# Kernel optimization log

Hardware: AMD Instinct MI355X
Metric: run time of the kernel (lower is better)

The kernel has to match this reference:

```python
import jax, jax.numpy as jnp
import numpy as np

CM = 8        # channel_mult
EPS = 1e-5    # BatchNorm eps
NEG = 0.2     # LeakyReLU slope


def conv2d(x, w, stride, pad, b=None):
    y = jax.lax.conv_general_dilated(
        x, w, (stride, stride), [(pad, pad), (pad, pad)],
        dimension_numbers=('NCHW', 'OIHW', 'NCHW'))
    if b is not None:
        y = y + b[None, :, None, None]
    return y


def per_sample_conv(x, w, stride, pad):
    # x: [B,C,H,W], w: [B,O,C,kh,kw] -> per-sample conv, vmapped over batch
    f = lambda xi, wi: conv2d(xi[None], wi, stride, pad)[0]
    return jax.vmap(f)(x, w)


def batchnorm(x, g, b):
    # training-mode BN: batch statistics over (N,H,W)
    m = jnp.mean(x, axis=(0, 2, 3), keepdims=True)
    v = jnp.var(x, axis=(0, 2, 3), keepdims=True)
    return (x - m) * jax.lax.rsqrt(v + EPS) * g[None, :, None, None] + b[None, :, None, None]


def lrelu(x):
    return jnp.where(x >= 0, x, NEG * x)


def setup_inputs() -> dict:
    key = jax.random.key(0)
    ks = jax.random.split(key, 16)
    B, H, W = 16, 512, 512

    def rn(k, shape, fan_in):
        return jax.random.normal(k, shape, jnp.float32) * np.float32(1.0 / np.sqrt(fan_in))

    inp = {}
    inp['x'] = jax.random.normal(ks[0], (B, 3, H, W), jnp.float32)
    n_meta = 3 * (CM // 2) * 25 + CM * (CM * 2 // 2) * 25  # 300 + 1600 = 1900
    inp['conv_weights'] = jax.random.normal(ks[1], (B, n_meta), jnp.float32) * 0.05
    inp['w11'] = rn(ks[2], (CM // 2, 3, 5, 5), 3 * 25)
    inp['b11'] = jnp.zeros((CM // 2,), jnp.float32)
    inp['w12'] = rn(ks[3], (CM * 2 // 2, CM, 5, 5), CM * 25)
    inp['b12'] = jnp.zeros((CM * 2 // 2,), jnp.float32)
    inp['bn1_g'] = jnp.ones((CM * 2,), jnp.float32)
    inp['bn1_b'] = jnp.zeros((CM * 2,), jnp.float32)
    # conv2 stack: (in, out, kernel)
    chans = [(CM * 2, CM * 4, 5), (CM * 4, CM * 8, 5), (CM * 8, CM * 16, 3), (CM * 16, CM * 16, 3)]
    for i, (ci, co, k) in enumerate(chans, 1):
        inp[f'c2w{i}'] = rn(ks[3 + i], (co, ci, k, k), ci * k * k)
        inp[f'c2b{i}'] = jnp.zeros((co,), jnp.float32)
        inp[f'bn{i}g'] = jnp.ones((co,), jnp.float32)
        inp[f'bn{i}b'] = jnp.zeros((co,), jnp.float32)
    return inp


def reference(x, conv_weights, w11, b11, w12, b12, bn1_g, bn1_b,
              c2w1, c2b1, bn1g, bn1b, c2w2, c2b2, bn2g, bn2b,
              c2w3, c2b3, bn3g, bn3b, c2w4, c2b4, bn4g, bn4b):
    B, _, H, W = x.shape
    n1 = 3 * (CM // 2) * 25
    w1 = conv_weights[:, :n1].reshape(B, CM // 2, 3, 5, 5)
    w2 = conv_weights[:, n1:].reshape(B, CM * 2 // 2, CM, 5, 5)

    # meta layer 1: shared half + per-sample dynamic half
    xx = conv2d(x, w11, 1, 2, b11)                  # [B, cm/2, H, W]
    half = per_sample_conv(x, w1, 1, 2)             # [B, cm/2, H, W]
    h = lrelu(jnp.concatenate([xx, half], axis=1))  # [B, cm, H, W]

    # meta layer 2 (stride 2)
    xx = conv2d(h, w12, 2, 2, b12)                  # [B, cm, H/2, W/2]
    half = per_sample_conv(h, w2, 2, 2)             # [B, cm, H/2, W/2]
    h = lrelu(batchnorm(jnp.concatenate([xx, half], axis=1), bn1_g, bn1_b))

    # dense conv stack
    for w_, b_, g_, be_, p in [
        (c2w1, c2b1, bn1g, bn1b, 2),
        (c2w2, c2b2, bn2g, bn2b, 2),
        (c2w3, c2b3, bn3g, bn3b, 1),
        (c2w4, c2b4, bn4g, bn4b, 1),
    ]:
        h = lrelu(batchnorm(conv2d(h, w_, 2, p, b_), g_, be_))

    return h.reshape(-1, CM * 16, H // 32, W // 32)
```

## Files before the change

kernel.cpp:

```cpp
#include <hip/hip_runtime.h>


typedef __attribute__((ext_vector_type(8))) short short8v;
typedef __attribute__((ext_vector_type(4))) float float4v;
typedef unsigned short u16;

#define LRELU_NEG 0.2f
#define BN_EPS 1e-5f

__device__ __forceinline__ float bf2f(u16 u){ union{unsigned i; float f;} v; v.i=(unsigned)u<<16; return v.f; }
__device__ __forceinline__ u16 f2bf(float f){ unsigned x=__float_as_uint(f); x += 0x7FFFu + ((x>>16)&1u); return (u16)(x>>16); }
__device__ __forceinline__ float lrelu(float v){ return v<0.f? LRELU_NEG*v : v; }

__device__ __forceinline__ void packw(int i, const float* __restrict__ w, u16* __restrict__ dst,
                                      int IC, int OC, int KSZ, int CPR) {
  int kq = i & 31, oc = (i>>5) % OC, c = i/(OC*32);
  int ky = c / CPR, r = c % CPR;
  int kk = r*32 + kq; int kx = kk / IC, ic = kk % IC;
  float v = (kx < KSZ) ? w[(((size_t)oc*IC + ic)*KSZ + ky)*KSZ + kx] : 0.f;
  dst[i] = f2bf(v);
}

__global__ __launch_bounds__(256) void prep_all(
    const float* __restrict__ w11, const float* __restrict__ w12,
    const float* __restrict__ b12, const float* __restrict__ cw,
    const float* __restrict__ wc1, const float* __restrict__ wc2,
    const float* __restrict__ wc3, const float* __restrict__ wc4,
    u16* __restrict__ wl1d, u16* __restrict__ wl2m, float* __restrict__ bl2,
    u16* __restrict__ d1, u16* __restrict__ d2, u16* __restrict__ d3, u16* __restrict__ d4,
    u16* __restrict__ h1) {
  int i = blockIdx.x*256 + threadIdx.x;
  if (i < 16) {
    bl2[i] = (i<8)? b12[i] : 0.f;
  } else if (i < 49168) {
    int j = i - 16;
    int b = j / 3072, r = j % 3072;
    int c = r >> 9, r2 = r & 511;
    int row = r2 >> 5, kk = r2 & 31;
    int kx = kk >> 2, ic = kk & 3;
    int grp = row >> 3, oc = row & 7;
    int ky = c - grp;
    float v = 0.f;
    if (ic < 3 && kx < 5 && ky >= 0 && ky < 5)
      v = (oc < 4) ? w11[((oc*3+ic)*5+ky)*5+kx]
                   : cw[b*1900 + (oc-4)*75 + ic*25 + ky*5 + kx];
    wl1d[j] = f2bf(v);
  } else if (i < 131088) {
    int j = i - 49168;
    int kq = j & 31, oc = (j>>5) & 15, c = (j>>9) % 10, b = j / 5120;
    int ky = c >> 1, r = c & 1;
    int kk = r*32 + kq; int kx = kk >> 3, ic = kk & 7;
    float v = 0.f;
    if (kx < 5)
      v = (oc < 8) ? w12[((oc*8+ic)*5+ky)*5+kx]
                   : cw[b*1900 + 300 + ((oc-8)*8+ic)*25 + ky*5 + kx];
    wl2m[j] = f2bf(v);
  } else if (i < 196880) {
    int j = i - 131088;
    int b = j / 4112, p = j % 4112;
    int y, xx;
    if (p < 2064) { int r = p/516; y = (r<2)? r : 512+r; xx = p%516; }
    else          { int q = p-2064; int cidx = q&3; xx = (cidx<2)? cidx : 512+cidx; y = 2 + (q>>2); }
    short8v z = {0,0,0,0,0,0,0,0};
    *(short8v*)(h1 + ((((size_t)b*516 + y)*2 + (xx&1))*258 + (xx>>1))*8) = z;
  } else if (i < 484624) {
    int j = i - 196880;
    if (j < 15360) packw(j, wc1, d1, 16, 32, 5, 3);
    else if (j < 66560) packw(j-15360, wc2, d2, 32, 64, 5, 5);
    else if (j < 140288) packw(j-66560, wc3, d3, 64, 128, 3, 6);
    else packw(j-140288, wc4, d4, 128, 128, 3, 12);
  }
}

__global__ __launch_bounds__(256) void conv_l1(const float* __restrict__ x,
    const u16* __restrict__ wl1d, const float* __restrict__ b11,
    u16* __restrict__ h1) {
  __shared__ __align__(16) u16 sx[20*72*4 + 32];
  const int tid = threadIdx.x, b = blockIdx.z;
  const int x0 = (blockIdx.x & 7) * 64;
  const int r0 = (blockIdx.x >> 3) * 16;

  if (tid < 32) sx[20*72*4 + tid] = 0;

  const bool interior = (r0 >= 16) & (r0 <= 480) & (x0 >= 64) & (x0 <= 384);
  if (interior) {
    for (int e = tid; e < 360; e += 256) {
      int row = e / 18, cg = e % 18;
      size_t base = ((size_t)b*3*512 + r0 + row - 2)*512 + x0 + cg*4 - 4;
      float4v p0 = *(const float4v*)(x + base);
      float4v p1 = *(const float4v*)(x + base + 262144);
      float4v p2 = *(const float4v*)(x + base + 524288);
      short8v lo, hi;
#pragma unroll
      for (int j = 0; j < 2; j++) {
        lo[4*j+0] = (short)f2bf(p0[j]);   lo[4*j+1] = (short)f2bf(p1[j]);
        lo[4*j+2] = (short)f2bf(p2[j]);   lo[4*j+3] = 0;
        hi[4*j+0] = (short)f2bf(p0[j+2]); hi[4*j+1] = (short)f2bf(p1[j+2]);
        hi[4*j+2] = (short)f2bf(p2[j+2]); hi[4*j+3] = 0;
      }
      u16* dp = sx + (row*72 + cg*4)*4;
      *(short8v*)dp = lo;
      *(short8v*)(dp + 8) = hi;
    }
  } else {
    for (int e = tid; e < 1440; e += 256) {
      int row = e / 72, col = e % 72;
      int gy = r0 + row - 2, gx = x0 + col - 4;
      float v0 = 0.f, v1 = 0.f, v2 = 0.f;
      if (gy >= 0 && gy < 512 && gx >= 0 && gx < 512) {
        size_t base = ((size_t)b*3*512 + gy)*512 + gx;
        v0 = x[base]; v1 = x[base + 262144]; v2 = x[base + 524288];
      }
      ushort4 pk = {f2bf(v0), f2bf(v1), f2bf(v2), 0};
      *(ushort4*)(sx + e*4) = pk;
    }
  }
  __syncthreads();

  const int lane = tid & 63, w = tid >> 6;
  const int l15 = lane & 15, sub = lane >> 4;

  short8v Wf[6];
  const u16* wb = wl1d + (size_t)b*3072;
#pragma unroll
  for (int c = 0; c < 6; c++)
    Wf[c] = *(const short8v*)(wb + (c*16 + l15)*32 + sub*8);

  float bvv[4];
#pragma unroll
  for (int r = 0; r < 4; r++) bvv[r] = (sub & 1) ? 0.f : b11[r];

  const int colb = w*16 + l15;
  const int rsel = sub >> 1;
  const int x_out = x0 + colb + 2;
  const int xpar = x_out & 1, xp = x_out >> 1;

#pragma unroll
  for (int p = 0; p < 8; p++) {
    float4v acc = {0.f, 0.f, 0.f, 0.f};
#pragma unroll
    for (int c = 0; c < 6; c++) {
      const u16* ap = sx + (((2*p + c)*72 + colb + 2) << 2) + sub*8;
      union { unsigned long long q[2]; short8v v; } ua;
      ua.q[0] = *(const unsigned long long*)(ap);
      ua.q[1] = *(const unsigned long long*)(ap + 4);
      acc = __builtin_amdgcn_mfma_f32_16x16x32_bf16(Wf[c], ua.v, acc, 0, 0, 0);
    }
    union { unsigned long long q; u16 h[4]; } mine;
#pragma unroll
    for (int r = 0; r < 4; r++) mine.h[r] = f2bf(lrelu(acc[r] + bvv[r]));
    unsigned long long other = __shfl_xor((long long)mine.q, 16);
    if (!(sub & 1)) {
      int outrow = r0 + 2*p + rsel;
      u16* dst = h1 + ((((size_t)b*516 + outrow + 2)*2 + xpar)*258 + xp)*8;
      union { unsigned long long q[2]; short8v v; } pk;
      pk.q[0] = mine.q; pk.q[1] = other;
      *(short8v*)dst = pk.v;
    }
  }
}

#define LOADC(cc, Ax, Bx) do {                                                   \
    const int ky_ = (cc) / CPR, r_ = (cc) % CPR;                                 \
    const int kk0_ = r_*32 + sub*8;                                              \
    const int kx_ = kk0_ / IC, ico_ = kk0_ % IC;                                 \
    const int t_ = kx_ + PADOFF;                                                 \
    _Pragma("unroll") for (int n_ = 0; n_ < WN; n_++)                            \
      Bx[n_] = *(const short8v*)(wbase + ((size_t)(cc)*OC + oc0 + n_*16 + l15)*32 + sub*8); \
    _Pragma("unroll") for (int f_ = 0; f_ < WM; f_++) {                          \
      int iy_ = 2*oyf[f_] + ky_ + PADOFF;                                        \
      Ax[f_] = *(const short8v*)(inb + (((size_t)iy_*2 + (t_&1))*IPWH + axb[f_] + (t_>>1))*IC + ico_); \
    }                                                                            \
  } while(0)

#define MFMAC(Ax, Bx) do {                                                       \
    _Pragma("unroll") for (int f_ = 0; f_ < WM; f_++)                            \
      _Pragma("unroll") for (int n_ = 0; n_ < WN; n_++)                          \
        acc[f_][n_] = __builtin_amdgcn_mfma_f32_16x16x32_bf16(Ax[f_], Bx[n_], acc[f_][n_], 0, 0, 0); \
  } while(0)

template <int IC, int OC, int KSZ, int S, int P, int CPR, int NCH,
          int IPH, int IPW, int OWL, int OPH, int OPW,
          int WM, int WN, int WVM, int WVN, bool PERS>
__global__ __launch_bounds__(WVM*WVN*64) void conv_mfma(
    const u16* __restrict__ in, const u16* __restrict__ wmfma,
    const float* __restrict__ bias, u16* __restrict__ out,
    float2* __restrict__ part2) {
  constexpr int OW = 1 << OWL;
  constexpr int PADOFF = 2 - P;
  constexpr int IPWH = IPW / 2;
  constexpr int OPWH = OPW / 2;
  const int tid = threadIdx.x, lane = tid & 63;
  const int w = tid >> 6, wm = w % WVM, wn = w / WVM;
  const int l15 = lane & 15, sub = lane >> 4;
  const int b = blockIdx.z;
  const int px0 = blockIdx.x * (16*WM*WVM) + wm * (16*WM);
  const int oc0 = blockIdx.y * (16*WN*WVN) + wn * (16*WN);

  int oyf[WM], oxb[WM], axb[WM];
#pragma unroll
  for (int f = 0; f < WM; f++) {
    int p = px0 + f*16;
    oyf[f] = p >> OWL;
    oxb[f] = p & (OW-1);
    axb[f] = oxb[f] + l15;
  }
  const u16* inb = in + (size_t)b*IPH*IPW*IC;
  const u16* wbase = wmfma + (PERS ? (size_t)b*NCH*OC*32 : (size_t)0);

  float4v acc[WM][WN];
#pragma unroll
  for (int f = 0; f < WM; f++)
#pragma unroll
    for (int n = 0; n < WN; n++) acc[f][n] = (float4v){0.f,0.f,0.f,0.f};

  constexpr int NC = KSZ * CPR;
  short8v A0[WM], B0[WN], A1[WM], B1[WN];
  LOADC(0, A0, B0);
#pragma unroll
  for (int c = 0; c < NC; c += 2) {
    if (c + 1 < NC) LOADC(c + 1, A1, B1);
    MFMAC(A0, B0);
    if (c + 2 < NC) LOADC(c + 2, A0, B0);
    if (c + 1 < NC) MFMAC(A1, B1);
  }

  float s[WN], q[WN];
#pragma unroll
  for (int n = 0; n < WN; n++) { s[n] = 0.f; q[n] = 0.f; }
#pragma unroll
  for (int f = 0; f < WM; f++) {
    const int oxs = oxb[f] + sub*4;
    const size_t rowb2 = ((size_t)b*OPH + oyf[f] + 2)*2;
#pragma unroll
    for (int n = 0; n < WN; n++) {
      int oc = oc0 + n*16 + l15;
      float bv = bias[oc];
#pragma unroll
      for (int rr = 0; rr < 4; rr++) {
        float v = acc[f][n][rr] + bv;
        int x_out = oxs + rr + 2;
        out[((rowb2 + (x_out & 1))*OPWH + (x_out >> 1))*OC + oc] = f2bf(v);
        s[n] += v; q[n] += v*v;
      }
    }
  }
#pragma unroll
  for (int n = 0; n < WN; n++) {
    s[n] += __shfl_xor(s[n], 16); s[n] += __shfl_xor(s[n], 32);
    q[n] += __shfl_xor(q[n], 16); q[n] += __shfl_xor(q[n], 32);
  }
  __shared__ float sred[WVM*WVN][WN][16][2];
  if (sub == 0) {
#pragma unroll
    for (int n = 0; n < WN; n++) { sred[w][n][l15][0] = s[n]; sred[w][n][l15][1] = q[n]; }
  }
  __syncthreads();
  const int NBp = gridDim.x * gridDim.z;
  const int pb = blockIdx.z * gridDim.x + blockIdx.x;
  const int tot = WVN*WN*16;
  if (tid < tot) {
    int c16 = tid & 15, n = (tid >> 4) % WN, wn2 = tid / (16*WN);
    float S_ = 0.f, Q_ = 0.f;
    for (int wm2 = 0; wm2 < WVM; wm2++) {
      S_ += sred[wn2*WVM + wm2][n][c16][0];
      Q_ += sred[wn2*WVM + wm2][n][c16][1];
    }
    int c = blockIdx.y*(16*WN*WVN) + wn2*(16*WN) + n*16 + c16;
    part2[(size_t)c*NBp + pb] = make_float2(S_, Q_);
  }
}

__global__ void bn_stage2(const float2* __restrict__ part2, const float* __restrict__ g,
                          const float* __restrict__ bb, float* __restrict__ stats,
                          int NBp, float invN) {
  int c = blockIdx.x;
  float s = 0.f, q = 0.f;
  for (int i = threadIdx.x; i < NBp; i += 64) {
    float2 p = part2[(size_t)c*NBp + i];
    s += p.x; q += p.y;
  }
  for (int o = 32; o > 0; o >>= 1) { s += __shfl_down(s, o); q += __shfl_down(q, o); }
  if (threadIdx.x == 0) {
    float m = s * invN;
    float var = q * invN - m*m;
    float sc = g[c] * rsqrtf(var + BN_EPS);
    stats[2*c] = sc;
    stats[2*c+1] = bb[c] - m*sc;
  }
}

template <int C, int PH, int PW, int HH, int WW>
__global__ __launch_bounds__(256) void bn_fin(u16* __restrict__ y, const float* __restrict__ stats,
                                              int total8) {
  int i = blockIdx.x*256 + threadIdx.x;
  if (i >= total8) return;
  size_t e = (size_t)i*8;
  int c0 = (int)(e & (C-1));
  int px = (int)(e / C);
  int xp = px % (PW/2);
  int t2 = px / (PW/2);
  int yy = (t2 >> 1) % PH;
  bool interior = (yy >= 2) & (yy < 2+HH) & (xp >= 1) & (xp <= WW/2);
  short8v u = *(short8v*)(y + e);
  short8v o;
#pragma unroll
  for (int j = 0; j < 8; j++) {
    float v = bf2f((u16)u[j]) * stats[2*(c0+j)] + stats[2*(c0+j)+1];
    o[j] = interior ? (short)f2bf(lrelu(v)) : (short)0;
  }
  *(short8v*)(y + e) = o;
}

__global__ __launch_bounds__(256) void out_k(const u16* __restrict__ y6,
                                             const float* __restrict__ stats,
                                             float* __restrict__ out) {
  int i = blockIdx.x*256 + threadIdx.x;
  if (i >= 131072) return;
  size_t e = (size_t)i*4;
  int c0 = (int)(e & 127);
  int px = (int)(e >> 7);
  int loc = px & 255, b = px >> 8;
  int y = loc >> 4, x = loc & 15;
  int xi = x + 2;
  const u16* src = y6 + ((((size_t)b*20 + y + 2)*2 + (xi & 1))*10 + (xi >> 1))*128 + c0;
  ushort4 u = *(const ushort4*)src;
  float vv[4] = {bf2f(u.x), bf2f(u.y), bf2f(u.z), bf2f(u.w)};
#pragma unroll
  for (int j = 0; j < 4; j++) {
    int c = c0 + j;
    float v = vv[j] * stats[2*c] + stats[2*c+1];
    out[(((size_t)b*128 + c) << 8) + loc] = lrelu(v);
  }
}

extern "C" void kernel_launch(void* const* d_in, const int* in_sizes, int n_in,
                              void* d_out, int out_size, void* d_ws, size_t ws_size,
                              hipStream_t stream) {
  const float* x    = (const float*)d_in[0];
  const float* cw   = (const float*)d_in[1];
  const float* w11  = (const float*)d_in[2];
  const float* b11  = (const float*)d_in[3];
  const float* w12  = (const float*)d_in[4];
  const float* b12  = (const float*)d_in[5];
  const float* bn1g = (const float*)d_in[6];
  const float* bn1b = (const float*)d_in[7];
  const float* c2w[4] = {(const float*)d_in[8], (const float*)d_in[12],
                         (const float*)d_in[16], (const float*)d_in[20]};
  const float* c2b[4] = {(const float*)d_in[9], (const float*)d_in[13],
                         (const float*)d_in[17], (const float*)d_in[21]};
  const float* bng[4] = {(const float*)d_in[10], (const float*)d_in[14],
                         (const float*)d_in[18], (const float*)d_in[22]};
  const float* bnb[4] = {(const float*)d_in[11], (const float*)d_in[15],
                         (const float*)d_in[19], (const float*)d_in[23]};

  char* ws = (char*)d_ws;
  u16* h1   = (u16*)(ws);
  u16* y3   = (u16*)(ws);
  u16* y4   = (u16*)(ws + 17842176);
  u16* y5   = (u16*)(ws + 27312128);
  u16* y6   = (u16*)(ws + 32620544);
  u16* yT2  = (u16*)(ws + 68158464);
  u16* wl2m = (u16*)(ws + 102769664);
  float* bl2    = (float*)(ws + 102933504);
  float2* part2 = (float2*)(ws + 102933568);
  float* stats2 = (float*)(ws + 103457856);
  float* stats3 = stats2 + 32;
  float* stats4 = stats3 + 64;
  float* stats5 = stats4 + 128;
  float* stats6 = stats5 + 256;
  u16* wl1d = (u16*)(ws + 103460800);
  u16* wS1  = (u16*)(ws + 103559104);
  u16* wS2  = (u16*)(ws + 103589824);
  u16* wS3  = (u16*)(ws + 103692224);
  u16* wS4  = (u16*)(ws + 103839680);

  prep_all<<<1894, 256, 0, stream>>>(w11, w12, b12, cw,
                                     c2w[0], c2w[1], c2w[2], c2w[3],
                                     wl1d, wl2m, bl2, wS1, wS2, wS3, wS4, h1);

  conv_l1<<<dim3(256, 1, 16), 256, 0, stream>>>(x, wl1d, b11, h1);

  conv_mfma<8,16,5,2,2, 2,10, 516,516, 8, 260,260, 4,1,4,1, true>
      <<<dim3(256,1,16), 256, 0, stream>>>(h1, wl2m, bl2, yT2, part2);

  bn_stage2<<<16, 64, 0, stream>>>(part2, bn1g, bn1b, stats2, 4096, 1.f/1048576.f);
  bn_fin<16,260,260,256,256><<<8450, 256, 0, stream>>>(yT2, stats2, 2163200);

  conv_mfma<16,32,5,2,2, 3,15, 260,260, 7, 132,132, 2,2,4,1, false>
      <<<dim3(128,1,16), 256, 0, stream>>>(yT2, wS1, c2b[0], y3, part2);
  bn_stage2<<<32, 64, 0, stream>>>(part2, bng[0], bnb[0], stats3, 2048, 1.f/262144.f);
  bn_fin<32,132,132,128,128><<<4356, 256, 0, stream>>>(y3, stats3, 1115136);

  conv_mfma<32,64,5,2,2, 5,25, 132,132, 6, 68,68, 2,2,2,2, false>
      <<<dim3(64,1,16), 256, 0, stream>>>(y3, wS2, c2b[1], y4, part2);
  bn_stage2<<<64, 64, 0, stream>>>(part2, bng[1], bnb[1], stats4, 1024, 1.f/65536.f);
  bn_fin<64,68,68,64,64><<<2312, 256, 0, stream>>>(y4, stats4, 591872);

  conv_mfma<64,128,3,2,1, 6,18, 68,68, 5, 36,36, 2,2,2,2, false>
      <<<dim3(16,2,16), 256, 0, stream>>>(y4, wS3, c2b[2], y5, part2);
  bn_stage2<<<128, 64, 0, stream>>>(part2, bng[2], bnb[2], stats5, 256, 1.f/16384.f);
  bn_fin<128,36,36,32,32><<<1296, 256, 0, stream>>>(y5, stats5, 331776);

  conv_mfma<128,128,3,2,1, 12,36, 36,36, 4, 20,20, 2,2,1,2, false>
      <<<dim3(8,2,16), 128, 0, stream>>>(y5, wS4, c2b[3], y6, part2);
  bn_stage2<<<128, 64, 0, stream>>>(part2, bng[3], bnb[3], stats6, 128, 1.f/4096.f);

  out_k<<<512, 256, 0, stream>>>(y6, stats6, (float*)d_out);
}
```

Measured before the change: 252.2 us.

## Fuse meta conv layers 1 and 2 into one kernel via shared-memory h1 tile

Merges the first per-sample conv and the stride-2 second conv into a single kernel. Each block computes a halo-padded 36x80 tile of the 8-channel layer-1 activation in LDS and consumes it directly for layer 2, also producing the BN partial sums. This removes the full-resolution h1 round trip through global memory, one launch, and the padding-zero pass in prep. In exchange it recomputes halo rows and columns of layer 1 and uses more LDS per 512-thread block, which may lower occupancy.

```diff
diff --git a/kernel.cpp b/kernel.cpp
--- a/kernel.cpp
+++ b/kernel.cpp
@@ -27,8 +27,7 @@
     const float* __restrict__ wc1, const float* __restrict__ wc2,
     const float* __restrict__ wc3, const float* __restrict__ wc4,
     u16* __restrict__ wl1d, u16* __restrict__ wl2m, float* __restrict__ bl2,
-    u16* __restrict__ d1, u16* __restrict__ d2, u16* __restrict__ d3, u16* __restrict__ d4,
-    u16* __restrict__ h1) {
+    u16* __restrict__ d1, u16* __restrict__ d2, u16* __restrict__ d3, u16* __restrict__ d4) {
   int i = blockIdx.x*256 + threadIdx.x;
   if (i < 16) {
     bl2[i] = (i<8)? b12[i] : 0.f;
@@ -55,16 +54,8 @@
       v = (oc < 8) ? w12[((oc*8+ic)*5+ky)*5+kx]
                    : cw[b*1900 + 300 + ((oc-8)*8+ic)*25 + ky*5 + kx];
     wl2m[j] = f2bf(v);
-  } else if (i < 196880) {
+  } else if (i < 418832) {
     int j = i - 131088;
-    int b = j / 4112, p = j % 4112;
-    int y, xx;
-    if (p < 2064) { int r = p/516; y = (r<2)? r : 512+r; xx = p%516; }
-    else          { int q = p-2064; int cidx = q&3; xx = (cidx<2)? cidx : 512+cidx; y = 2 + (q>>2); }
-    short8v z = {0,0,0,0,0,0,0,0};
-    *(short8v*)(h1 + ((((size_t)b*516 + y)*2 + (xx&1))*258 + (xx>>1))*8) = z;
-  } else if (i < 484624) {
-    int j = i - 196880;
     if (j < 15360) packw(j, wc1, d1, 16, 32, 5, 3);
     else if (j < 66560) packw(j-15360, wc2, d2, 32, 64, 5, 5);
     else if (j < 140288) packw(j-66560, wc3, d3, 64, 128, 3, 6);
@@ -72,21 +63,24 @@
   }
 }
 
-__global__ __launch_bounds__(256) void conv_l1(const float* __restrict__ x,
+__global__ __launch_bounds__(512) void conv_l12(const float* __restrict__ x,
     const u16* __restrict__ wl1d, const float* __restrict__ b11,
-    u16* __restrict__ h1) {
-  __shared__ __align__(16) u16 sx[20*72*4 + 32];
+    const u16* __restrict__ wl2m, const float* __restrict__ bl2,
+    u16* __restrict__ yT2, float2* __restrict__ part2) {
+  __shared__ __align__(16) u16 sx[40*88*4];
+  __shared__ __align__(16) u16 sh1[36*2*40*8];
+  __shared__ float sred[8][16][2];
+
   const int tid = threadIdx.x, b = blockIdx.z;
-  const int x0 = (blockIdx.x & 7) * 64;
-  const int r0 = (blockIdx.x >> 3) * 16;
-
-  if (tid < 32) sx[20*72*4 + tid] = 0;
-
-  const bool interior = (r0 >= 16) & (r0 <= 480) & (x0 >= 64) & (x0 <= 384);
+  const int tx = blockIdx.x & 7, ty = blockIdx.x >> 3;
+  const int x0 = tx*32, y0 = ty*16;
+  const int xg0 = 2*x0 - 4, yg0 = 2*y0 - 4;
+
+  const bool interior = (xg0 >= 0) & (xg0 + 87 < 512) & (yg0 >= 0) & (yg0 + 39 < 512);
   if (interior) {
-    for (int e = tid; e < 360; e += 256) {
-      int row = e / 18, cg = e % 18;
-      size_t base = ((size_t)b*3*512 + r0 + row - 2)*512 + x0 + cg*4 - 4;
+    for (int e = tid; e < 880; e += 512) {
+      int row = e / 22, cg = e % 22;
+      size_t base = ((size_t)b*3*512 + yg0 + row)*512 + xg0 + cg*4;
       float4v p0 = *(const float4v*)(x + base);
       float4v p1 = *(const float4v*)(x + base + 262144);
       float4v p2 = *(const float4v*)(x + base + 524288);
@@ -98,14 +92,14 @@
         hi[4*j+0] = (short)f2bf(p0[j+2]); hi[4*j+1] = (short)f2bf(p1[j+2]);
         hi[4*j+2] = (short)f2bf(p2[j+2]); hi[4*j+3] = 0;
       }
-      u16* dp = sx + (row*72 + cg*4)*4;
+      u16* dp = sx + (row*88 + cg*4)*4;
       *(short8v*)dp = lo;
       *(short8v*)(dp + 8) = hi;
     }
   } else {
-    for (int e = tid; e < 1440; e += 256) {
-      int row = e / 72, col = e % 72;
-      int gy = r0 + row - 2, gx = x0 + col - 4;
+    for (int e = tid; e < 3520; e += 512) {
+      int row = e / 88, col = e % 88;
+      int gy = yg0 + row, gx = xg0 + col;
       float v0 = 0.f, v1 = 0.f, v2 = 0.f;
       if (gy >= 0 && gy < 512 && gx >= 0 && gx < 512) {
         size_t base = ((size_t)b*3*512 + gy)*512 + gx;
@@ -117,46 +111,92 @@
   }
   __syncthreads();
 
-  const int lane = tid & 63, w = tid >> 6;
+  const int lane = tid & 63, wid = tid >> 6;
   const int l15 = lane & 15, sub = lane >> 4;
 
-  short8v Wf[6];
-  const u16* wb = wl1d + (size_t)b*3072;
-#pragma unroll
-  for (int c = 0; c < 6; c++)
-    Wf[c] = *(const short8v*)(wb + (c*16 + l15)*32 + sub*8);
-
-  float bvv[4];
-#pragma unroll
-  for (int r = 0; r < 4; r++) bvv[r] = (sub & 1) ? 0.f : b11[r];
-
-  const int colb = w*16 + l15;
-  const int rsel = sub >> 1;
-  const int x_out = x0 + colb + 2;
-  const int xpar = x_out & 1, xp = x_out >> 1;
-
-#pragma unroll
-  for (int p = 0; p < 8; p++) {
-    float4v acc = {0.f, 0.f, 0.f, 0.f};
-#pragma unroll
-    for (int c = 0; c < 6; c++) {
-      const u16* ap = sx + (((2*p + c)*72 + colb + 2) << 2) + sub*8;
-      union { unsigned long long q[2]; short8v v; } ua;
-      ua.q[0] = *(const unsigned long long*)(ap);
-      ua.q[1] = *(const unsigned long long*)(ap + 4);
-      acc = __builtin_amdgcn_mfma_f32_16x16x32_bf16(Wf[c], ua.v, acc, 0, 0, 0);
-    }
-    union { unsigned long long q; u16 h[4]; } mine;
-#pragma unroll
-    for (int r = 0; r < 4; r++) mine.h[r] = f2bf(lrelu(acc[r] + bvv[r]));
-    unsigned long long other = __shfl_xor((long long)mine.q, 16);
-    if (!(sub & 1)) {
-      int outrow = r0 + 2*p + rsel;
-      u16* dst = h1 + ((((size_t)b*516 + outrow + 2)*2 + xpar)*258 + xp)*8;
-      union { unsigned long long q[2]; short8v v; } pk;
-      pk.q[0] = mine.q; pk.q[1] = other;
-      *(short8v*)dst = pk.v;
-    }
+  {
+    short8v Wf[6];
+    const u16* wb = wl1d + (size_t)b*3072;
+#pragma unroll
+    for (int c = 0; c < 6; c++)
+      Wf[c] = *(const short8v*)(wb + (c*16 + l15)*32 + sub*8);
+    float bvv[4];
+#pragma unroll
+    for (int r = 0; r < 4; r++) bvv[r] = (sub & 1) ? 0.f : b11[r];
+    const int rsel = sub >> 1, ch0 = (sub & 1)*4;
+
+    for (int t = wid; t < 90; t += 8) {
+      int s = t % 5, p = t / 5;
+      int colb = s*16 + l15;
+      float4v acc = {0.f, 0.f, 0.f, 0.f};
+#pragma unroll
+      for (int c = 0; c < 6; c++) {
+        const u16* ap = sx + (((2*p + c)*88 + colb) << 2) + sub*8;
+        union { unsigned long long q[2]; short8v v; } ua;
+        ua.q[0] = *(const unsigned long long*)(ap);
+        ua.q[1] = *(const unsigned long long*)(ap + 4);
+        acc = __builtin_amdgcn_mfma_f32_16x16x32_bf16(Wf[c], ua.v, acc, 0, 0, 0);
+      }
+      int r_l = 2*p + rsel;
+      int hr = 2*y0 - 2 + r_l;
+      int hc = 2*x0 - 2 + colb;
+      bool valid = (hr >= 0) & (hr < 512) & (hc >= 0) & (hc < 512);
+      union { unsigned long long q; u16 h[4]; } mine;
+#pragma unroll
+      for (int r = 0; r < 4; r++)
+        mine.h[r] = valid ? f2bf(lrelu(acc[r] + bvv[r])) : (u16)0;
+      *(unsigned long long*)(sh1 + ((r_l*2 + (colb & 1))*40 + (colb >> 1))*8 + ch0) = mine.q;
+    }
+  }
+  __syncthreads();
+
+  const u16* w2 = wl2m + (size_t)b*5120;
+  float4v acc2[4];
+  int oyl[4], oxl[4];
+#pragma unroll
+  for (int j = 0; j < 4; j++) {
+    int t2 = wid*4 + j;
+    oyl[j] = t2 >> 1;
+    oxl[j] = (t2 & 1)*16;
+    acc2[j] = (float4v){0.f, 0.f, 0.f, 0.f};
+  }
+#pragma unroll
+  for (int c = 0; c < 10; c++) {
+    int ky = c >> 1, r = c & 1;
+    int kx = r*4 + sub;
+    short8v B = *(const short8v*)(w2 + ((size_t)c*16 + l15)*32 + sub*8);
+#pragma unroll
+    for (int j = 0; j < 4; j++) {
+      int rowl = 2*oyl[j] + ky;
+      int pos = oxl[j] + l15 + (kx >> 1);
+      short8v A = *(const short8v*)(sh1 + ((rowl*2 + (kx & 1))*40 + pos)*8);
+      acc2[j] = __builtin_amdgcn_mfma_f32_16x16x32_bf16(A, B, acc2[j], 0, 0, 0);
+    }
+  }
+
+  float s_ = 0.f, q_ = 0.f;
+  const float bv = bl2[l15];
+#pragma unroll
+  for (int j = 0; j < 4; j++) {
+    const size_t rowb2 = ((size_t)b*260 + y0 + oyl[j] + 2)*2;
+    const int oxs = x0 + oxl[j] + sub*4;
+#pragma unroll
+    for (int rr = 0; rr < 4; rr++) {
+      float v = acc2[j][rr] + bv;
+      int x_out = oxs + rr + 2;
+      yT2[((rowb2 + (x_out & 1))*130 + (x_out >> 1))*16 + l15] = f2bf(v);
+      s_ += v; q_ += v*v;
+    }
+  }
+  s_ += __shfl_xor(s_, 16); s_ += __shfl_xor(s_, 32);
+  q_ += __shfl_xor(q_, 16); q_ += __shfl_xor(q_, 32);
+  if (sub == 0) { sred[wid][l15][0] = s_; sred[wid][l15][1] = q_; }
+  __syncthreads();
+  if (tid < 16) {
+    float S_ = 0.f, Q_ = 0.f;
+#pragma unroll
+    for (int w2i = 0; w2i < 8; w2i++) { S_ += sred[w2i][tid][0]; Q_ += sred[w2i][tid][1]; }
+    part2[(size_t)tid*2048 + b*128 + blockIdx.x] = make_float2(S_, Q_);
   }
 }
 
@@ -355,7 +395,6 @@
                          (const float*)d_in[19], (const float*)d_in[23]};
 
   char* ws = (char*)d_ws;
-  u16* h1   = (u16*)(ws);
   u16* y3   = (u16*)(ws);
   u16* y4   = (u16*)(ws + 17842176);
   u16* y5   = (u16*)(ws + 27312128);
@@ -375,16 +414,13 @@
   u16* wS3  = (u16*)(ws + 103692224);
   u16* wS4  = (u16*)(ws + 103839680);
 
-  prep_all<<<1894, 256, 0, stream>>>(w11, w12, b12, cw,
+  prep_all<<<1637, 256, 0, stream>>>(w11, w12, b12, cw,
                                      c2w[0], c2w[1], c2w[2], c2w[3],
-                                     wl1d, wl2m, bl2, wS1, wS2, wS3, wS4, h1);
-
-  conv_l1<<<dim3(256, 1, 16), 256, 0, stream>>>(x, wl1d, b11, h1);
-
-  conv_mfma<8,16,5,2,2, 2,10, 516,516, 8, 260,260, 4,1,4,1, true>
-      <<<dim3(256,1,16), 256, 0, stream>>>(h1, wl2m, bl2, yT2, part2);
-
-  bn_stage2<<<16, 64, 0, stream>>>(part2, bn1g, bn1b, stats2, 4096, 1.f/1048576.f);
+                                     wl1d, wl2m, bl2, wS1, wS2, wS3, wS4);
+
+  conv_l12<<<dim3(128, 1, 16), 512, 0, stream>>>(x, wl1d, b11, wl2m, bl2, yT2, part2);
+
+  bn_stage2<<<16, 64, 0, stream>>>(part2, bn1g, bn1b, stats2, 2048, 1.f/1048576.f);
   bn_fin<16,260,260,256,256><<<8450, 256, 0, stream>>>(yT2, stats2, 2163200);
 
   conv_mfma<16,32,5,2,2, 3,15, 260,260, 7, 132,132, 2,2,4,1, false>
```

Result: faster. 230.2 us (-8.7%).
